# Kernel tuning notes

Hardware: AMD Instinct MI355X
Metric: run time of the kernel (lower is better)

The kernel has to match this reference:

```python
import jax, jax.numpy as jnp
import numpy as np

TEMPERATURE = 10000.0
LN_EPS = 1e-5

def build_freqs(H, W, head_dim):
    # (H*W, head_dim) rotary angles: [theta_h, theta_h, theta_w, theta_w]
    gh, gw = jnp.meshgrid(jnp.arange(H, dtype=jnp.float32), jnp.arange(W, dtype=jnp.float32), indexing='ij')
    dq = head_dim // 4
    freq = 1.0 / (TEMPERATURE ** (jnp.arange(dq, dtype=jnp.float32) / dq))
    th = gh.reshape(-1, 1) * freq[None, :]
    tw = gw.reshape(-1, 1) * freq[None, :]
    return jnp.concatenate([th, th, tw, tw], axis=-1)

def apply_rope(x, freqs):
    # x: (B, nh, N, hd), freqs: (N, hd)
    cos = jnp.cos(freqs)[None, None]
    sin = jnp.sin(freqs)[None, None]
    hd = x.shape[-1]
    x1, x2 = x[..., :hd // 2], x[..., hd // 2:]
    x_rot = jnp.concatenate([-x2, x1], axis=-1)
    return x * cos + x_rot * sin

def setup_inputs() -> dict:
    key = jax.random.key(0)
    ks = jax.random.split(key, 8)
    dim, hidden, B, H, W = 192, 384, 4, 128, 128
    N = H * W
    s = 0.02
    return {
        'x': jax.random.normal(ks[0], (B, N, dim), jnp.float32),
        'in_w': jax.random.normal(ks[1], (hidden, dim), jnp.float32) * s,
        'in_b': jnp.zeros((hidden,), jnp.float32),
        'qkv_w': jax.random.normal(ks[2], (3 * hidden, hidden), jnp.float32) * s,
        'qkv_b': jnp.zeros((3 * hidden,), jnp.float32),
        'lepe_w': jax.random.normal(ks[3], (hidden, 1, 3, 3), jnp.float32) * s,
        'lepe_b': jnp.zeros((hidden,), jnp.float32),
        'ln_g': jnp.ones((hidden,), jnp.float32),
        'ln_b': jnp.zeros((hidden,), jnp.float32),
        'out_w': jax.random.normal(ks[4], (dim, hidden), jnp.float32) * s,
        'out_b': jnp.zeros((dim,), jnp.float32),
        'H': H,
        'W': W,
    }

def reference(x, in_w, in_b, qkv_w, qkv_b, lepe_w, lepe_b, ln_g, ln_b, out_w, out_b, H, W):
    B, N, C = x.shape
    hidden = in_w.shape[0]
    nh = 8
    hd = hidden // nh
    # in_proj: 1x1 conv == per-token linear
    x_seq = jnp.einsum('bnc,hc->bnh', x, in_w) + in_b
    # fused qkv
    qkv = jnp.einsum('bnh,oh->bno', x_seq, qkv_w) + qkv_b
    q, k, v = jnp.split(qkv, 3, axis=-1)
    # LEPE: 3x3 depthwise conv on V in NCHW layout
    v2d = v.transpose(0, 2, 1).reshape(B, hidden, H, W)
    lepe = jax.lax.conv_general_dilated(
        v2d, lepe_w, window_strides=(1, 1), padding=((1, 1), (1, 1)),
        feature_group_count=hidden, dimension_numbers=('NCHW', 'OIHW', 'NCHW'))
    lepe = lepe + lepe_b[None, :, None, None]
    v = v + lepe.reshape(B, hidden, N).transpose(0, 2, 1)
    # split heads -> (B, nh, N, hd)
    q = q.reshape(B, N, nh, hd).transpose(0, 2, 1, 3)
    k = k.reshape(B, N, nh, hd).transpose(0, 2, 1, 3)
    v = v.reshape(B, N, nh, hd).transpose(0, 2, 1, 3)
    freqs = build_freqs(H, W, hd)
    q = apply_rope(q, freqs)
    k = apply_rope(k, freqs)
    # phi = ELU + 1 feature map
    q = jax.nn.elu(q) + 1.0
    k = jax.nn.elu(k) + 1.0
    # linear attention associativity trick
    kv = jnp.einsum('bhnd,bhne->bhde', k, v)
    out = jnp.einsum('bhnd,bhde->bhne', q, kv)
    k_sum = k.sum(axis=2)  # (B, nh, hd)
    denom = jnp.maximum(jnp.einsum('bhnd,bhd->bhn', q, k_sum)[..., None], 1e-6)
    out = out / denom
    out = out.transpose(0, 2, 1, 3).reshape(B, N, hidden)
    # LayerNorm + out_proj
    mu = out.mean(axis=-1, keepdims=True)
    var = out.var(axis=-1, keepdims=True)
    out = (out - mu) * jax.lax.rsqrt(var + LN_EPS) * ln_g + ln_b
    return jnp.einsum('bnh,ch->bnc', out, out_w) + out_b
```

## Files before the change

### kernel.cpp

```cpp
#include <hip/hip_runtime.h>
#include <cstdint>
#include <cstddef>

#define NN_TOK 16384
#define ROWS   65536
#define CDIM   192
#define HID    384
#define NHEAD  8
#define HD     48
#define QKVO   1152

typedef unsigned short ushort_t;
typedef __bf16 bf16x8 __attribute__((ext_vector_type(8)));
typedef float  f32x4  __attribute__((ext_vector_type(4)));

__device__ __forceinline__ ushort_t f2bf(float f) {
  unsigned int u = __float_as_uint(f);
  u += 0x7fffu + ((u >> 16) & 1u);
  return (ushort_t)(u >> 16);
}
__device__ __forceinline__ float bf2f(ushort_t u) {
  return __uint_as_float(((unsigned int)u) << 16);
}

__global__ void cast_x(const float* __restrict__ x, ushort_t* __restrict__ xb, int n8) {
  int i = blockIdx.x * blockDim.x + threadIdx.x;
  if (i >= n8) return;
  const float4* src = (const float4*)(x + (size_t)i * 8);
  float4 f0 = src[0], f1 = src[1];
  uint4 pk;
  pk.x = (unsigned)f2bf(f0.x) | ((unsigned)f2bf(f0.y) << 16);
  pk.y = (unsigned)f2bf(f0.z) | ((unsigned)f2bf(f0.w) << 16);
  pk.z = (unsigned)f2bf(f1.x) | ((unsigned)f2bf(f1.y) << 16);
  pk.w = (unsigned)f2bf(f1.z) | ((unsigned)f2bf(f1.w) << 16);
  *(uint4*)(xb + (size_t)i * 8) = pk;
}

__global__ void combine_w(const float* __restrict__ in_w, const float* __restrict__ in_b,
                          const float* __restrict__ qkv_w, const float* __restrict__ qkv_b,
                          ushort_t* __restrict__ Wcb, float* __restrict__ bc) {
  int o = blockIdx.x;
  int c = threadIdx.x;
  const float* qw = qkv_w + o * HID;
  float s = 0.f;
  for (int m = 0; m < HID; ++m) s += qw[m] * in_w[m * CDIM + c];
  Wcb[o * CDIM + c] = f2bf(s);
  if (c == 0) {
    float sb = qkv_b[o];
    for (int m = 0; m < HID; ++m) sb += qw[m] * in_b[m];
    bc[o] = sb;
  }
}

__global__ void cast_ow(const float* __restrict__ w, ushort_t* __restrict__ wb, int n) {
  int i = blockIdx.x * blockDim.x + threadIdx.x;
  if (i < n) wb[i] = f2bf(w[i]);
}

__global__ void build_tab(float4* __restrict__ tab4) {
  int i = blockIdx.x * blockDim.x + threadIdx.x;
  if (i >= NN_TOK * 24) return;
  int n = i / 24, dp = i - n * 24;
  int j = dp % 12;
  const float c0 = 1.1073093649624542f;
  float freq = exp2f(-(float)j * c0);
  float fy = (float)(n >> 7), fx = (float)(n & 127);
  float s1, c1, s2, c2;
  sincosf(fy * freq, &s1, &c1);
  sincosf(fx * freq, &s2, &c2);
  tab4[i] = make_float4(c1, s1, c2, s2);
}

template<int BM, int BN, int WM, int WN, bool OUTBF16>
__global__ __launch_bounds__(256) void gemm_mfma(const ushort_t* __restrict__ A, int lda,
                                                 const ushort_t* __restrict__ Wb,
                                                 const float* __restrict__ bias,
                                                 void* __restrict__ Cptr,
                                                 int K, int O) {
  constexpr int TM = BM / WM / 16;
  constexpr int TN = BN / WN / 16;
  __shared__ __align__(16) ushort_t As[BM][40];
  __shared__ __align__(16) ushort_t Bs[BN][40];
  const int t    = threadIdx.x;
  const int lane = t & 63;
  const int wave = t >> 6;
  const int quad = lane >> 4;
  const int l15  = lane & 15;
  const int wm   = wave / WN, wn = wave % WN;
  const int m_base = wm * (BM / WM);
  const int n_base = wn * (BN / WN);
  const int n0 = blockIdx.y * BM;
  const int o0 = blockIdx.x * BN;
  f32x4 acc[TM][TN] = {};

  for (int kt = 0; kt < K; kt += 32) {
    for (int c = t; c < BM * 4; c += 256) {
      int row = c >> 2, col8 = (c & 3) * 8;
      *(uint4*)&As[row][col8] = *(const uint4*)(A + (size_t)(n0 + row) * lda + kt + col8);
    }
    for (int c = t; c < BN * 4; c += 256) {
      int row = c >> 2, col8 = (c & 3) * 8;
      *(uint4*)&Bs[row][col8] = *(const uint4*)(Wb + (size_t)(o0 + row) * K + kt + col8);
    }
    __syncthreads();
    bf16x8 af[TM], bfr[TN];
#pragma unroll
    for (int mi = 0; mi < TM; ++mi)
      af[mi] = *(const bf16x8*)&As[m_base + mi * 16 + l15][quad * 8];
#pragma unroll
    for (int ni = 0; ni < TN; ++ni)
      bfr[ni] = *(const bf16x8*)&Bs[n_base + ni * 16 + l15][quad * 8];
#pragma unroll
    for (int mi = 0; mi < TM; ++mi)
#pragma unroll
      for (int ni = 0; ni < TN; ++ni)
        acc[mi][ni] = __builtin_amdgcn_mfma_f32_16x16x32_bf16(af[mi], bfr[ni], acc[mi][ni], 0, 0, 0);
    __syncthreads();
  }
#pragma unroll
  for (int mi = 0; mi < TM; ++mi) {
#pragma unroll
    for (int ni = 0; ni < TN; ++ni) {
      int col = o0 + n_base + ni * 16 + l15;
      float bv = bias[col];
      int rbase = n0 + m_base + mi * 16 + quad * 4;
#pragma unroll
      for (int r = 0; r < 4; ++r) {
        float val = acc[mi][ni][r] + bv;
        if (OUTBF16) ((ushort_t*)Cptr)[(size_t)(rbase + r) * O + col] = f2bf(val);
        else         ((float*)Cptr)[(size_t)(rbase + r) * O + col] = val;
      }
    }
  }
}

__global__ __launch_bounds__(256) void kv_partial_k(const ushort_t* __restrict__ kq,
                                                    const ushort_t* __restrict__ vq,
                                                    const float4* __restrict__ tab4,
                                                    const float* __restrict__ lw,
                                                    const float* __restrict__ lb,
                                                    float* __restrict__ part) {
  const int bid   = blockIdx.x;
  const int chunk = bid & 63;
  const int bh    = bid >> 6;
  const int b     = bh >> 3;
  const int h     = bh & 7;
  const int t     = threadIdx.x;
  const int lane  = t & 63;
  const int wave  = t >> 6;
  __shared__ __align__(16) ushort_t ksF[3][16][16][8];
  __shared__ __align__(16) ushort_t vsF[3][16][16][8];
  __shared__ float wlds[9][48];
  __shared__ float blds[48];
  float* red   = (float*)&ksF[0][0][0][0];
  float* ksred = (float*)&vsF[0][0][0][0];
  for (int c = t; c < 432; c += 256) {
    int ch = c / 9, tap = c - ch * 9;
    wlds[tap][ch] = lw[(h * HD + ch) * 9 + tap];
  }
  if (t < 48) blds[t] = lb[h * HD + t];
  __syncthreads();

  const int g  = lane >> 4;
  const int d0 = lane & 15;
  f32x4 acc[3][3] = {};
  float ksacc = 0.f;
  const int n0 = b * NN_TOK + chunk * 256;

  for (int it = 0; it < 2; ++it) {
    const int nbase = it * 128;
    for (int c = t; c < 384; c += 256) {
      int rr = c / 3, s8 = (c - (c / 3) * 3) * 8;
      int n  = n0 + nbase + rr;
      int nn = n & (NN_TOK - 1);
      const ushort_t* kr = kq + (size_t)n * QKVO + h * HD;
      uint4 ka = *(const uint4*)(kr + s8);
      uint4 kb = *(const uint4*)(kr + s8 + 24);
      ushort_t ua[8], ub[8];
      *(uint4*)ua = ka; *(uint4*)ub = kb;
      const float4* t4 = tab4 + nn * 24 + s8;
      const int nb = rr >> 3, nm = rr & 7;
#pragma unroll
      for (int jj = 0; jj < 8; ++jj) {
        float4 cs = t4[jj];
        float in1 = bf2f(ua[jj]), in2 = bf2f(ub[jj]);
        float o1 = in1 * cs.x - in2 * cs.y;
        float o2 = in2 * cs.z + in1 * cs.w;
        o1 = (o1 > 0.f) ? o1 + 1.f : expf(o1);
        o2 = (o2 > 0.f) ? o2 + 1.f : expf(o2);
        const int d1 = s8 + jj, d2 = s8 + 24 + jj;
        ksF[d1 >> 4][nb][d1 & 15][nm] = f2bf(o1);
        ksF[d2 >> 4][nb][d2 & 15][nm] = f2bf(o2);
      }
    }
    {
      const int nst = chunk * 256 + nbase;
      const int y   = nst >> 7;
      for (int c = t; c < 768; c += 256) {
        int rr = c / 6, gg = c - (c / 6) * 6;
        int x = rr;
        float a8[8], ctr[8];
#pragma unroll
        for (int ci = 0; ci < 8; ++ci) a8[ci] = blds[gg * 8 + ci];
#pragma unroll
        for (int dy = -1; dy <= 1; ++dy) {
#pragma unroll
          for (int dx = -1; dx <= 1; ++dx) {
            int yy = y + dy, xx = x + dx;
            float m = ((unsigned)yy < 128u && (unsigned)xx < 128u) ? 1.f : 0.f;
            int yc = min(max(yy, 0), 127), xc = min(max(xx, 0), 127);
            const ushort_t* src = vq + ((size_t)(b * NN_TOK + (yc << 7) + xc)) * QKVO + h * HD + gg * 8;
            uint4 pk = *(const uint4*)src;
            ushort_t uu[8];
            *(uint4*)uu = pk;
            const int tap = (dy + 1) * 3 + (dx + 1);
#pragma unroll
            for (int ci = 0; ci < 8; ++ci) {
              float val = bf2f(uu[ci]);
              if (dy == 0 && dx == 0) ctr[ci] = val;
              a8[ci] += (wlds[tap][gg * 8 + ci] * m) * val;
            }
          }
        }
        const int nb = rr >> 3, nm = rr & 7;
#pragma unroll
        for (int ci = 0; ci < 8; ++ci) {
          const int e = gg * 8 + ci;
          vsF[e >> 4][nb][e & 15][nm] = f2bf(ctr[ci] + a8[ci]);
        }
      }
    }
    __syncthreads();
    {
      const int w4 = wave * 4 + g;
      bf16x8 af[3], bfr[3];
#pragma unroll
      for (int dg = 0; dg < 3; ++dg) af[dg]  = *(const bf16x8*)&ksF[dg][w4][d0][0];
#pragma unroll
      for (int eg = 0; eg < 3; ++eg) bfr[eg] = *(const bf16x8*)&vsF[eg][w4][d0][0];
#pragma unroll
      for (int dg = 0; dg < 3; ++dg)
#pragma unroll
        for (int eg = 0; eg < 3; ++eg)
          acc[dg][eg] = __builtin_amdgcn_mfma_f32_16x16x32_bf16(af[dg], bfr[eg], acc[dg][eg], 0, 0, 0);
    }
    if (lane < 48) {
      const int dg = lane >> 4, dd = lane & 15;
#pragma unroll 8
      for (int rr = 0; rr < 32; ++rr) {
        int nl = wave * 32 + rr;
        ksacc += bf2f(ksF[dg][nl >> 3][dd][nl & 7]);
      }
    }
    __syncthreads();
  }
  if (wave == 0) {
#pragma unroll
    for (int dg = 0; dg < 3; ++dg)
#pragma unroll
      for (int eg = 0; eg < 3; ++eg)
#pragma unroll
        for (int r = 0; r < 4; ++r)
          red[(dg * 16 + g * 4 + r) * 48 + eg * 16 + d0] = acc[dg][eg][r];
  }
  if (lane < 48) ksred[wave * 48 + lane] = ksacc;
  __syncthreads();
  for (int w = 1; w < 4; ++w) {
    if (wave == w) {
#pragma unroll
      for (int dg = 0; dg < 3; ++dg)
#pragma unroll
        for (int eg = 0; eg < 3; ++eg)
#pragma unroll
          for (int r = 0; r < 4; ++r)
            red[(dg * 16 + g * 4 + r) * 48 + eg * 16 + d0] += acc[dg][eg][r];
    }
    __syncthreads();
  }
  float* p = part + (size_t)bid * 2352;
  for (int c = t; c < 2304; c += 256) p[c] = red[c];
  if (t < 48) p[2304 + t] = ksred[t] + ksred[48 + t] + ksred[96 + t] + ksred[144 + t];
}

__global__ void kv_phase2(const float* __restrict__ part, float* __restrict__ kvb,
                          float* __restrict__ ksum) {
  int bh  = blockIdx.x >> 3;
  int seg = blockIdx.x & 7;
  int t   = threadIdx.x;
  int cend = (seg + 1) * 294;
  for (int c = seg * 294 + t; c < cend; c += 256) {
    const float* p = part + (size_t)(bh * 64) * 2352 + c;
    float s = 0.f;
    for (int ch = 0; ch < 64; ++ch) s += p[(size_t)ch * 2352];
    if (c < 2304) kvb[bh * 2304 + c] = s;
    else          ksum[bh * 48 + (c - 2304)] = s;
  }
}

__global__ __launch_bounds__(256) void attn_ln_fused(const ushort_t* __restrict__ q,
                                                     const float4* __restrict__ tab4,
                                                     const float* __restrict__ kvg,
                                                     const float* __restrict__ ksum,
                                                     const float* __restrict__ ln_g,
                                                     const float* __restrict__ ln_b,
                                                     ushort_t* __restrict__ oln) {
  __shared__ __align__(16) float qs[32][8][52];
  __shared__ float denomS[32][8];
  const int t    = threadIdx.x;
  const int row0 = blockIdx.x * 32;
  const int b    = row0 >> 14;
  for (int c = t; c < 1536; c += 256) {
    int r = c / 48, g = c - (c / 48) * 48;
    int h = g / 6, d = (g - h * 6) * 8;
    uint4 pk = *(const uint4*)(q + (size_t)(row0 + r) * QKVO + g * 8);
    ushort_t uu[8];
    *(uint4*)uu = pk;
    *(float4*)&qs[r][h][d]     = make_float4(bf2f(uu[0]), bf2f(uu[1]), bf2f(uu[2]), bf2f(uu[3]));
    *(float4*)&qs[r][h][d + 4] = make_float4(bf2f(uu[4]), bf2f(uu[5]), bf2f(uu[6]), bf2f(uu[7]));
  }
  __syncthreads();
  {
    int r = t >> 3, h = t & 7;
    int n = (row0 + r) & (NN_TOK - 1);
    const float4* t4 = tab4 + n * 24;
    const float* ksh = ksum + (b * 8 + h) * 48;
    float dn = 0.f;
#pragma unroll 4
    for (int dp = 0; dp < 24; ++dp) {
      float4 cs = t4[dp];
      float in1 = qs[r][h][dp], in2 = qs[r][h][dp + 24];
      float o1 = in1 * cs.x - in2 * cs.y;
      float o2 = in2 * cs.z + in1 * cs.w;
      o1 = (o1 > 0.f) ? o1 + 1.f : expf(o1);
      o2 = (o2 > 0.f) ? o2 + 1.f : expf(o2);
      qs[r][h][dp]      = o1;
      qs[r][h][dp + 24] = o2;
      dn += o1 * ksh[dp] + o2 * ksh[dp + 24];
    }
    denomS[r][h] = fmaxf(dn, 1e-6f);
  }
  __syncthreads();
  const int lane = t & 63, rg = t >> 6;
  const int hh = lane >> 3;
  const int e0 = (lane & 7) * 6;
  const float* kvh = kvg + (size_t)(b * 8 + hh) * 48 * 48;
  float acc[8][6] = {};
#pragma unroll 2
  for (int d = 0; d < 48; ++d) {
    float kvv[6];
    *(float2*)&kvv[0] = *(const float2*)(kvh + d * 48 + e0);
    *(float2*)&kvv[2] = *(const float2*)(kvh + d * 48 + e0 + 2);
    *(float2*)&kvv[4] = *(const float2*)(kvh + d * 48 + e0 + 4);
#pragma unroll
    for (int i = 0; i < 8; ++i) {
      float qv = qs[rg * 8 + i][hh][d];
#pragma unroll
      for (int j = 0; j < 6; ++j) acc[i][j] += qv * kvv[j];
    }
  }
  float gg[6], bb[6];
#pragma unroll
  for (int j = 0; j < 6; ++j) {
    gg[j] = ln_g[lane * 6 + j];
    bb[j] = ln_b[lane * 6 + j];
  }
#pragma unroll
  for (int i = 0; i < 8; ++i) {
    int r = rg * 8 + i;
    float dnm = denomS[r][hh];
    float o[6];
    float s = 0.f, sq = 0.f;
#pragma unroll
    for (int j = 0; j < 6; ++j) {
      o[j] = acc[i][j] / dnm;
      s += o[j]; sq += o[j] * o[j];
    }
#pragma unroll
    for (int m = 1; m < 64; m <<= 1) {
      s  += __shfl_xor(s, m, 64);
      sq += __shfl_xor(sq, m, 64);
    }
    float mu   = s * (1.f / 384.f);
    float var  = sq * (1.f / 384.f) - mu * mu;
    float rstd = rsqrtf(var + 1e-5f);
    unsigned pk0 = (unsigned)f2bf((o[0] - mu) * rstd * gg[0] + bb[0]) |
                   ((unsigned)f2bf((o[1] - mu) * rstd * gg[1] + bb[1]) << 16);
    unsigned pk1 = (unsigned)f2bf((o[2] - mu) * rstd * gg[2] + bb[2]) |
                   ((unsigned)f2bf((o[3] - mu) * rstd * gg[3] + bb[3]) << 16);
    unsigned pk2 = (unsigned)f2bf((o[4] - mu) * rstd * gg[4] + bb[4]) |
                   ((unsigned)f2bf((o[5] - mu) * rstd * gg[5] + bb[5]) << 16);
    unsigned* dst = (unsigned*)(oln + (size_t)(row0 + r) * QKVO + lane * 6);
    dst[0] = pk0; dst[1] = pk1; dst[2] = pk2;
  }
}

extern "C" void kernel_launch(void* const* d_in, const int* in_sizes, int n_in,
                              void* d_out, int out_size, void* d_ws, size_t ws_size,
                              hipStream_t stream) {
  const float* x      = (const float*)d_in[0];
  const float* in_w   = (const float*)d_in[1];
  const float* in_b   = (const float*)d_in[2];
  const float* qkv_w  = (const float*)d_in[3];
  const float* qkv_b  = (const float*)d_in[4];
  const float* lepe_w = (const float*)d_in[5];
  const float* lepe_b = (const float*)d_in[6];
  const float* ln_g   = (const float*)d_in[7];
  const float* ln_b   = (const float*)d_in[8];
  const float* out_w  = (const float*)d_in[9];
  const float* out_b  = (const float*)d_in[10];
  float* out = (float*)d_out;

  float*    ws     = (float*)d_ws;
  float*    qkvbF  = ws;
  float*    xbF    = qkvbF + (size_t)ROWS * QKVO / 2;
  float*    WcbF   = xbF   + (size_t)ROWS * CDIM / 2;
  float*    bc     = WcbF  + (size_t)QKVO * CDIM / 2;
  float*    owbF   = bc    + QKVO;
  float*    kvb    = owbF  + (size_t)CDIM * HID / 2;
  float*    ksum   = kvb   + 32 * HD * HD;
  float*    tab4F  = ksum  + 32 * HD;
  ushort_t* qkvb   = (ushort_t*)qkvbF;
  ushort_t* xb     = (ushort_t*)xbF;
  float*    part   = xbF;
  ushort_t* Wcb    = (ushort_t*)WcbF;
  ushort_t* owb    = (ushort_t*)owbF;
  float4*   tab4   = (float4*)tab4F;

  cast_x<<<(ROWS * CDIM / 8 + 255) / 256, 256, 0, stream>>>(x, xb, ROWS * CDIM / 8);
  combine_w<<<QKVO, CDIM, 0, stream>>>(in_w, in_b, qkv_w, qkv_b, Wcb, bc);
  cast_ow<<<(CDIM * HID + 255) / 256, 256, 0, stream>>>(out_w, owb, CDIM * HID);
  build_tab<<<(NN_TOK * 24 + 255) / 256, 256, 0, stream>>>(tab4);

  dim3 gqkv(QKVO / 128, ROWS / 128);
  gemm_mfma<128, 128, 2, 2, true><<<gqkv, 256, 0, stream>>>(xb, CDIM, Wcb, bc, qkvb, CDIM, QKVO);

  kv_partial_k<<<2048, 256, 0, stream>>>(qkvb + HID, qkvb + 2 * HID, tab4, lepe_w, lepe_b, part);
  kv_phase2<<<256, 256, 0, stream>>>(part, kvb, ksum);

  attn_ln_fused<<<ROWS / 32, 256, 0, stream>>>(qkvb, tab4, kvb, ksum, ln_g, ln_b, qkvb + HID);

  dim3 g6(CDIM / 64, ROWS / 128);
  gemm_mfma<128, 64, 4, 1, false><<<g6, 256, 0, stream>>>(qkvb + HID, QKVO, owb, out_b, out, HID, CDIM);
}
```

Baseline: 447.8 us.

## Compute q·KV and denominator with bf16 MFMA using split hi/lo KV matrix

The attention-output kernel now computes q·KV on MFMA instead of scalar FP32 FMAs over shared memory. kv_phase2 writes a transposed, padded bf16 KV matrix split into hi and lo halves, with ksum appended as an extra column so the denominator falls out of the same MFMA. The LayerNorm reduction moves to cross-wave partial sums in shared memory. In exchange, feature-mapped q is rounded to bf16, which adds precision loss, and output stores become scattered 2-byte writes.

```diff
diff --git a/kernel.cpp b/kernel.cpp
--- a/kernel.cpp
+++ b/kernel.cpp
@@ -282,116 +282,190 @@
   if (t < 48) p[2304 + t] = ksred[t] + ksred[48 + t] + ksred[96 + t] + ksred[144 + t];
 }
 
-__global__ void kv_phase2(const float* __restrict__ part, float* __restrict__ kvb,
-                          float* __restrict__ ksum) {
+__global__ void kv_phase2(const float* __restrict__ part, ushort_t* __restrict__ kvT) {
   int bh  = blockIdx.x >> 3;
   int seg = blockIdx.x & 7;
   int t   = threadIdx.x;
+  ushort_t* dst = kvT + (size_t)bh * 8192;
+  for (int i = seg * 1024 + t; i < (seg + 1) * 1024; i += 256) {
+    int rem = i & 4095, e = rem >> 6, d = rem & 63;
+    if (d >= 48 || e >= 49) dst[i] = 0;
+  }
   int cend = (seg + 1) * 294;
   for (int c = seg * 294 + t; c < cend; c += 256) {
     const float* p = part + (size_t)(bh * 64) * 2352 + c;
     float s = 0.f;
     for (int ch = 0; ch < 64; ++ch) s += p[(size_t)ch * 2352];
-    if (c < 2304) kvb[bh * 2304 + c] = s;
-    else          ksum[bh * 48 + (c - 2304)] = s;
+    int d, e;
+    if (c < 2304) { d = c / 48; e = c - d * 48; }
+    else          { e = 48; d = c - 2304; }
+    ushort_t hi = f2bf(s);
+    float lo = s - bf2f(hi);
+    dst[(size_t)e * 64 + d]        = hi;
+    dst[4096 + (size_t)e * 64 + d] = f2bf(lo);
   }
 }
 
 __global__ __launch_bounds__(256) void attn_ln_fused(const ushort_t* __restrict__ q,
                                                      const float4* __restrict__ tab4,
-                                                     const float* __restrict__ kvg,
-                                                     const float* __restrict__ ksum,
+                                                     const ushort_t* __restrict__ kvT,
                                                      const float* __restrict__ ln_g,
                                                      const float* __restrict__ ln_b,
                                                      ushort_t* __restrict__ oln) {
-  __shared__ __align__(16) float qs[32][8][52];
-  __shared__ float denomS[32][8];
+  __shared__ float lnp[4][32][2];
   const int t    = threadIdx.x;
+  const int lane = t & 63;
+  const int wave = t >> 6;
+  const int quad = lane >> 4;
+  const int l15  = lane & 15;
   const int row0 = blockIdx.x * 32;
   const int b    = row0 >> 14;
-  for (int c = t; c < 1536; c += 256) {
-    int r = c / 48, g = c - (c / 48) * 48;
-    int h = g / 6, d = (g - h * 6) * 8;
-    uint4 pk = *(const uint4*)(q + (size_t)(row0 + r) * QKVO + g * 8);
-    ushort_t uu[8];
-    *(uint4*)uu = pk;
-    *(float4*)&qs[r][h][d]     = make_float4(bf2f(uu[0]), bf2f(uu[1]), bf2f(uu[2]), bf2f(uu[3]));
-    *(float4*)&qs[r][h][d + 4] = make_float4(bf2f(uu[4]), bf2f(uu[5]), bf2f(uu[6]), bf2f(uu[7]));
+  const int h0   = wave * 2;
+
+  f32x4 acc[2][2][4] = {};
+
+  float gg[2][3], bb[2][3];
+#pragma unroll
+  for (int hi = 0; hi < 2; ++hi)
+#pragma unroll
+    for (int nt = 0; nt < 3; ++nt) {
+      int col = (h0 + hi) * 48 + nt * 16 + l15;
+      gg[hi][nt] = ln_g[col];
+      bb[hi][nt] = ln_b[col];
+    }
+
+#pragma unroll
+  for (int s = 0; s < 2; ++s) {
+    const int d0 = s * 32 + quad * 8;
+    const bool valid = d0 < 48;
+    const bool caseA = d0 < 24;
+    const int dp0 = caseA ? d0 : d0 - 24;
+    bf16x8 af[2][2] = {};
+    if (valid) {
+      const int dpart = caseA ? d0 + 24 : d0 - 24;
+#pragma unroll
+      for (int m = 0; m < 2; ++m) {
+        const int r  = row0 + m * 16 + l15;
+        const int nn = r & (NN_TOK - 1);
+        const float4* t4 = tab4 + nn * 24 + dp0;
+        float4 cs[8];
+#pragma unroll
+        for (int j = 0; j < 8; ++j) cs[j] = t4[j];
+#pragma unroll
+        for (int hi = 0; hi < 2; ++hi) {
+          const ushort_t* qr = q + (size_t)r * QKVO + (h0 + hi) * 48;
+          uint4 pr = *(const uint4*)(qr + d0);
+          uint4 pa = *(const uint4*)(qr + dpart);
+          ushort_t up[8], ua[8];
+          *(uint4*)up = pr; *(uint4*)ua = pa;
+          unsigned w[4];
+#pragma unroll
+          for (int j2 = 0; j2 < 4; ++j2) {
+            float o2[2];
+#pragma unroll
+            for (int k = 0; k < 2; ++k) {
+              int j = j2 * 2 + k;
+              float vp = bf2f(up[j]), va = bf2f(ua[j]);
+              float c  = caseA ? cs[j].x : cs[j].z;
+              float sn = caseA ? -cs[j].y : cs[j].w;
+              float o = vp * c + va * sn;
+              o2[k] = (o > 0.f) ? o + 1.f : expf(o);
+            }
+            w[j2] = (unsigned)f2bf(o2[0]) | ((unsigned)f2bf(o2[1]) << 16);
+          }
+          uint4 pk = make_uint4(w[0], w[1], w[2], w[3]);
+          af[hi][m] = *(bf16x8*)&pk;
+        }
+      }
+    }
+#pragma unroll
+    for (int hi = 0; hi < 2; ++hi) {
+      const ushort_t* kb = kvT + (size_t)(b * 8 + h0 + hi) * 8192;
+#pragma unroll
+      for (int nt = 0; nt < 4; ++nt) {
+        bf16x8 bH = *(const bf16x8*)(kb + (nt * 16 + l15) * 64 + d0);
+        bf16x8 bL = *(const bf16x8*)(kb + 4096 + (nt * 16 + l15) * 64 + d0);
+#pragma unroll
+        for (int m = 0; m < 2; ++m) {
+          acc[hi][m][nt] = __builtin_amdgcn_mfma_f32_16x16x32_bf16(af[hi][m], bH, acc[hi][m][nt], 0, 0, 0);
+          acc[hi][m][nt] = __builtin_amdgcn_mfma_f32_16x16x32_bf16(af[hi][m], bL, acc[hi][m][nt], 0, 0, 0);
+        }
+      }
+    }
+  }
+
+  float rdn[2][2][4];
+#pragma unroll
+  for (int hi = 0; hi < 2; ++hi)
+#pragma unroll
+    for (int m = 0; m < 2; ++m)
+#pragma unroll
+      for (int r = 0; r < 4; ++r) {
+        float dn = __shfl(acc[hi][m][3][r], lane & 48);
+        rdn[hi][m][r] = 1.f / fmaxf(dn, 1e-6f);
+      }
+  float s1[2][4] = {}, s2[2][4] = {};
+#pragma unroll
+  for (int hi = 0; hi < 2; ++hi)
+#pragma unroll
+    for (int m = 0; m < 2; ++m)
+#pragma unroll
+      for (int nt = 0; nt < 3; ++nt)
+#pragma unroll
+        for (int r = 0; r < 4; ++r) {
+          float o = acc[hi][m][nt][r] * rdn[hi][m][r];
+          acc[hi][m][nt][r] = o;
+          s1[m][r] += o;
+          s2[m][r] += o * o;
+        }
+#pragma unroll
+  for (int m = 0; m < 2; ++m)
+#pragma unroll
+    for (int r = 0; r < 4; ++r) {
+#pragma unroll
+      for (int msk = 1; msk < 16; msk <<= 1) {
+        s1[m][r] += __shfl_xor(s1[m][r], msk, 64);
+        s2[m][r] += __shfl_xor(s2[m][r], msk, 64);
+      }
+    }
+  if (l15 == 0) {
+#pragma unroll
+    for (int m = 0; m < 2; ++m)
+#pragma unroll
+      for (int r = 0; r < 4; ++r) {
+        int rr = m * 16 + quad * 4 + r;
+        lnp[wave][rr][0] = s1[m][r];
+        lnp[wave][rr][1] = s2[m][r];
+      }
   }
   __syncthreads();
-  {
-    int r = t >> 3, h = t & 7;
-    int n = (row0 + r) & (NN_TOK - 1);
-    const float4* t4 = tab4 + n * 24;
-    const float* ksh = ksum + (b * 8 + h) * 48;
-    float dn = 0.f;
-#pragma unroll 4
-    for (int dp = 0; dp < 24; ++dp) {
-      float4 cs = t4[dp];
-      float in1 = qs[r][h][dp], in2 = qs[r][h][dp + 24];
-      float o1 = in1 * cs.x - in2 * cs.y;
-      float o2 = in2 * cs.z + in1 * cs.w;
-      o1 = (o1 > 0.f) ? o1 + 1.f : expf(o1);
-      o2 = (o2 > 0.f) ? o2 + 1.f : expf(o2);
-      qs[r][h][dp]      = o1;
-      qs[r][h][dp + 24] = o2;
-      dn += o1 * ksh[dp] + o2 * ksh[dp + 24];
-    }
-    denomS[r][h] = fmaxf(dn, 1e-6f);
-  }
-  __syncthreads();
-  const int lane = t & 63, rg = t >> 6;
-  const int hh = lane >> 3;
-  const int e0 = (lane & 7) * 6;
-  const float* kvh = kvg + (size_t)(b * 8 + hh) * 48 * 48;
-  float acc[8][6] = {};
-#pragma unroll 2
-  for (int d = 0; d < 48; ++d) {
-    float kvv[6];
-    *(float2*)&kvv[0] = *(const float2*)(kvh + d * 48 + e0);
-    *(float2*)&kvv[2] = *(const float2*)(kvh + d * 48 + e0 + 2);
-    *(float2*)&kvv[4] = *(const float2*)(kvh + d * 48 + e0 + 4);
-#pragma unroll
-    for (int i = 0; i < 8; ++i) {
-      float qv = qs[rg * 8 + i][hh][d];
-#pragma unroll
-      for (int j = 0; j < 6; ++j) acc[i][j] += qv * kvv[j];
-    }
-  }
-  float gg[6], bb[6];
-#pragma unroll
-  for (int j = 0; j < 6; ++j) {
-    gg[j] = ln_g[lane * 6 + j];
-    bb[j] = ln_b[lane * 6 + j];
-  }
-#pragma unroll
-  for (int i = 0; i < 8; ++i) {
-    int r = rg * 8 + i;
-    float dnm = denomS[r][hh];
-    float o[6];
-    float s = 0.f, sq = 0.f;
-#pragma unroll
-    for (int j = 0; j < 6; ++j) {
-      o[j] = acc[i][j] / dnm;
-      s += o[j]; sq += o[j] * o[j];
-    }
-#pragma unroll
-    for (int m = 1; m < 64; m <<= 1) {
-      s  += __shfl_xor(s, m, 64);
-      sq += __shfl_xor(sq, m, 64);
-    }
-    float mu   = s * (1.f / 384.f);
-    float var  = sq * (1.f / 384.f) - mu * mu;
-    float rstd = rsqrtf(var + 1e-5f);
-    unsigned pk0 = (unsigned)f2bf((o[0] - mu) * rstd * gg[0] + bb[0]) |
-                   ((unsigned)f2bf((o[1] - mu) * rstd * gg[1] + bb[1]) << 16);
-    unsigned pk1 = (unsigned)f2bf((o[2] - mu) * rstd * gg[2] + bb[2]) |
-                   ((unsigned)f2bf((o[3] - mu) * rstd * gg[3] + bb[3]) << 16);
-    unsigned pk2 = (unsigned)f2bf((o[4] - mu) * rstd * gg[4] + bb[4]) |
-                   ((unsigned)f2bf((o[5] - mu) * rstd * gg[5] + bb[5]) << 16);
-    unsigned* dst = (unsigned*)(oln + (size_t)(row0 + r) * QKVO + lane * 6);
-    dst[0] = pk0; dst[1] = pk1; dst[2] = pk2;
-  }
+  float muv[2][4], rsv[2][4];
+#pragma unroll
+  for (int m = 0; m < 2; ++m)
+#pragma unroll
+    for (int r = 0; r < 4; ++r) {
+      int rr = m * 16 + quad * 4 + r;
+      float a  = lnp[0][rr][0] + lnp[1][rr][0] + lnp[2][rr][0] + lnp[3][rr][0];
+      float bq = lnp[0][rr][1] + lnp[1][rr][1] + lnp[2][rr][1] + lnp[3][rr][1];
+      float mu  = a * (1.f / 384.f);
+      float var = bq * (1.f / 384.f) - mu * mu;
+      muv[m][r] = mu;
+      rsv[m][r] = rsqrtf(var + 1e-5f);
+    }
+#pragma unroll
+  for (int hi = 0; hi < 2; ++hi)
+#pragma unroll
+    for (int m = 0; m < 2; ++m)
+#pragma unroll
+      for (int nt = 0; nt < 3; ++nt) {
+        int col = (h0 + hi) * 48 + nt * 16 + l15;
+#pragma unroll
+        for (int r = 0; r < 4; ++r) {
+          int row = row0 + m * 16 + quad * 4 + r;
+          float v = (acc[hi][m][nt][r] - muv[m][r]) * rsv[m][r] * gg[hi][nt] + bb[hi][nt];
+          oln[(size_t)row * QKVO + col] = f2bf(v);
+        }
+      }
 }
 
 extern "C" void kernel_launch(void* const* d_in, const int* in_sizes, int n_in,
@@ -416,12 +490,11 @@
   float*    WcbF   = xbF   + (size_t)ROWS * CDIM / 2;
   float*    bc     = WcbF  + (size_t)QKVO * CDIM / 2;
   float*    owbF   = bc    + QKVO;
-  float*    kvb    = owbF  + (size_t)CDIM * HID / 2;
-  float*    ksum   = kvb   + 32 * HD * HD;
-  float*    tab4F  = ksum  + 32 * HD;
+  float*    tab4F  = owbF  + (size_t)CDIM * HID / 2;
   ushort_t* qkvb   = (ushort_t*)qkvbF;
   ushort_t* xb     = (ushort_t*)xbF;
   float*    part   = xbF;
+  ushort_t* kvT    = (ushort_t*)(xbF + (size_t)2048 * 2352);
   ushort_t* Wcb    = (ushort_t*)WcbF;
   ushort_t* owb    = (ushort_t*)owbF;
   float4*   tab4   = (float4*)tab4F;
@@ -435,9 +508,9 @@
   gemm_mfma<128, 128, 2, 2, true><<<gqkv, 256, 0, stream>>>(xb, CDIM, Wcb, bc, qkvb, CDIM, QKVO);
 
   kv_partial_k<<<2048, 256, 0, stream>>>(qkvb + HID, qkvb + 2 * HID, tab4, lepe_w, lepe_b, part);
-  kv_phase2<<<256, 256, 0, stream>>>(part, kvb, ksum);
-
-  attn_ln_fused<<<ROWS / 32, 256, 0, stream>>>(qkvb, tab4, kvb, ksum, ln_g, ln_b, qkvb + HID);
+  kv_phase2<<<256, 256, 0, stream>>>(part, kvT);
+
+  attn_ln_fused<<<ROWS / 32, 256, 0, stream>>>(qkvb, tab4, kvT, ln_g, ln_b, qkvb + HID);
 
   dim3 g6(CDIM / 64, ROWS / 128);
   gemm_mfma<128, 64, 4, 1, false><<<g6, 256, 0, stream>>>(qkvb + HID, QKVO, owb, out_b, out, HID, CDIM);
```

New measurement: 458.1 us. 2.3% more time.
